# Performance work log

Measured on AMD Instinct MI355X. Metric: run time of the kernel, lower is better.

Reference implementation:

```python
import jax, jax.numpy as jnp
import numpy as np

NUM_EMBEDDINGS = 1024
EMBEDDING_DIM = 256

def setup_inputs() -> dict:
    key = jax.random.key(0)
    k1, k2 = jax.random.split(key)
    x = jax.random.normal(k1, (8, 16, 32, 32, EMBEDDING_DIM), dtype=jnp.float32)
    embeddings = jax.random.normal(k2, (NUM_EMBEDDINGS, EMBEDDING_DIM), dtype=jnp.float32)
    return {"x": x, "embeddings": embeddings}

def reference(x, embeddings):
    # Flatten all leading dims to tokens: [N, D]
    flat = x.reshape(-1, EMBEDDING_DIM)
    # Squared euclidean distances via ||a||^2 + ||b||^2 - 2 a.b  -> [N, K]
    sim = jnp.matmul(flat, embeddings.T)
    distances = (jnp.sum(flat * flat, axis=1, keepdims=True)
                 + jnp.sum(embeddings * embeddings, axis=1)
                 - 2.0 * sim)
    encoding_indices = jnp.argmin(distances, axis=1)  # [N]
    quantized = embeddings[encoding_indices].reshape(x.shape)
    # Perplexity from code usage histogram (mean of one-hot == normalized counts)
    counts = jnp.zeros((NUM_EMBEDDINGS,), dtype=jnp.float32).at[encoding_indices].add(1.0)
    avg_probs = counts / flat.shape[0]
    perplexity = jnp.exp(-jnp.sum(avg_probs * jnp.log(avg_probs + 1e-10)))
    return quantized, perplexity
```

## Files before the change

kernel.cpp:

```cpp
#include <hip/hip_runtime.h>
#include <math.h>
#include <stdint.h>

#define NTOK 131072
#define DIM  256
#define KEMB 1024

typedef _Float16 f16x8 __attribute__((ext_vector_type(8)));
typedef float    f32x4 __attribute__((ext_vector_type(4)));

#define FLAG_CAP 65536
#define FLAG_THR 8u

static __device__ __forceinline__ unsigned umin32(unsigned a, unsigned b){ return a<b?a:b; }
static __device__ __forceinline__ unsigned umax32(unsigned a, unsigned b){ return a>b?a:b; }

static __device__ __forceinline__ void gload_lds16(const void* g, void* l) {
    __builtin_amdgcn_global_load_lds(
        (const __attribute__((address_space(1))) unsigned int*)g,
        (__attribute__((address_space(3))) unsigned int*)l, 16, 0, 0);
}

static __device__ __forceinline__ void split_hl(const float4& f0, const float4& f1,
                                                f16x8& h, f16x8& l) {
    float v[8] = {f0.x, f0.y, f0.z, f0.w, f1.x, f1.y, f1.z, f1.w};
    #pragma unroll
    for (int e = 0; e < 8; ++e) {
        const _Float16 hi = (_Float16)v[e];
        h[e] = hi;
        l[e] = (_Float16)(v[e] - (float)hi);
    }
}

__global__ __launch_bounds__(64) void prep_kernel(const float* __restrict__ emb,
                                                  float* __restrict__ eNorm,
                                                  float* __restrict__ cst2,
                                                  unsigned* __restrict__ counts,
                                                  unsigned* __restrict__ flagCnt,
                                                  _Float16* __restrict__ img_hi,
                                                  _Float16* __restrict__ img_lo) {
    const int k = blockIdx.x;
    const int lane = threadIdx.x;
    const float4 v = *reinterpret_cast<const float4*>(emb + (size_t)k * DIM + lane * 4);
    float s = v.x * v.x + v.y * v.y + v.z * v.z + v.w * v.w;
    #pragma unroll
    for (int m = 32; m; m >>= 1) s += __shfl_xor(s, m, 64);
    if (lane == 0) {
        eNorm[k] = s;
        cst2[k]  = s + 512.0f;
        counts[k] = 0u;
        if (k == 0) *flagCnt = 0u;
    }
    if (lane < 32) {
        const int p = lane;
        const int sl = p ^ (k & 7);
        const float4 f0 = *reinterpret_cast<const float4*>(emb + (size_t)k * DIM + sl * 8);
        const float4 f1 = *reinterpret_cast<const float4*>(emb + (size_t)k * DIM + sl * 8 + 4);
        f16x8 h, l;
        split_hl(f0, f1, h, l);
        *reinterpret_cast<f16x8*>(img_hi + (size_t)k * 256 + p * 8) = h;
        *reinterpret_cast<f16x8*>(img_lo + (size_t)k * 256 + p * 8) = l;
    }
}

__global__ __launch_bounds__(256, 2) void vq_main(const float* __restrict__ x,
                                                  const float* __restrict__ emb,
                                                  const _Float16* __restrict__ img,
                                                  const float* __restrict__ cst2,
                                                  int* __restrict__ idxArr,
                                                  unsigned* __restrict__ counts,
                                                  unsigned* __restrict__ flagCnt,
                                                  unsigned* __restrict__ flagList,
                                                  float* __restrict__ out) {
    __shared__ char Bsh[4][2][8192];
    __shared__ float cst_s[1024];
    __shared__ int idx_s[256];

    const int tid  = threadIdx.x;
    const int wv   = tid >> 6;
    const int lane = tid & 63;
    const int g    = lane >> 4;
    const int c    = lane & 15;
    const int T0   = blockIdx.x * 256;
    const int T0w  = T0 + wv * 64;

    char* const ldsbase = &Bsh[wv][0][0];

    *reinterpret_cast<float4*>(&cst_s[tid * 4]) =
        *reinterpret_cast<const float4*>(&cst2[tid * 4]);

    {
        const char* src = (const char*)img + lane * 16;
        #pragma unroll
        for (int i = 0; i < 8; ++i)
            gload_lds16(src + i * 1024, ldsbase + i * 1024);
    }

    f16x8 a[4][8];
    #pragma unroll
    for (int i = 0; i < 4; ++i) {
        const float* xr = x + (size_t)(T0w + i * 16 + c) * DIM + g * 8;
        #pragma unroll
        for (int kk = 0; kk < 8; ++kk) {
            const float4 f0 = *reinterpret_cast<const float4*>(xr + kk * 32);
            const float4 f1 = *reinterpret_cast<const float4*>(xr + kk * 32 + 4);
            a[i][kk] = (f16x8){(_Float16)f0.x, (_Float16)f0.y, (_Float16)f0.z, (_Float16)f0.w,
                               (_Float16)f1.x, (_Float16)f1.y, (_Float16)f1.z, (_Float16)f1.w};
        }
    }

    unsigned m1[16], m2[16];
    #pragma unroll
    for (int t = 0; t < 16; ++t) { m1[t] = 0xFFFFFFFFu; m2[t] = 0xFFFFFFFFu; }

    __syncthreads();

#define ISSUE(NXT, ECN) do {                                                   \
        const char* _src = (const char*)img + (size_t)(ECN) * 8192 + lane * 16;\
        char* _dst = ldsbase + (NXT) * 8192;                                   \
        _Pragma("unroll")                                                      \
        for (int _i = 0; _i < 8; ++_i)                                         \
            gload_lds16(_src + _i * 1024, _dst + _i * 1024);                   \
    } while (0)

#define COMPUTE(CUR, EC) do {                                                  \
        const _Float16* _B = (const _Float16*)(ldsbase + (CUR) * 8192);        \
        const int   _col = (EC) * 16 + c;                                      \
        const float _cst = cst_s[_col];                                        \
        f32x4 _acc[4];                                                         \
        _Pragma("unroll")                                                      \
        for (int _i = 0; _i < 4; ++_i) _acc[_i] = (f32x4){0.f, 0.f, 0.f, 0.f}; \
        __builtin_amdgcn_s_setprio(1);                                         \
        _Pragma("unroll")                                                      \
        for (int _kk = 0; _kk < 8; ++_kk) {                                    \
            const f16x8 _b = *reinterpret_cast<const f16x8*>(                  \
                _B + c * 256 + (((_kk * 4 + g) ^ (c & 7)) << 3));              \
            _Pragma("unroll")                                                  \
            for (int _i = 0; _i < 4; ++_i)                                     \
                _acc[_i] = __builtin_amdgcn_mfma_f32_16x16x32_f16(             \
                    a[_i][_kk], _b, _acc[_i], 0, 0, 0);                        \
        }                                                                      \
        __builtin_amdgcn_s_setprio(0);                                         \
        _Pragma("unroll")                                                      \
        for (int _i = 0; _i < 4; ++_i)                                         \
            _Pragma("unroll")                                                  \
            for (int _e = 0; _e < 4; ++_e) {                                   \
                const float    _d = fmaf(_acc[_i][_e], -2.0f, _cst);           \
                const unsigned _k = (__builtin_bit_cast(unsigned, _d)          \
                                     & 0xFFFFFC00u) | (unsigned)_col;          \
                const int _t = _i * 4 + _e;                                    \
                m2[_t] = umin32(m2[_t], umax32(_k, m1[_t]));                   \
                m1[_t] = umin32(m1[_t], _k);                                   \
            }                                                                  \
    } while (0)

    for (int ec2 = 0; ec2 < 32; ++ec2) {
        const int ec0 = ec2 * 2;
        const int ec1 = ec0 + 1;

        ISSUE(1, ec0 + 1);
        asm volatile("s_waitcnt vmcnt(8)" ::: "memory");
        __builtin_amdgcn_sched_barrier(0);
        COMPUTE(0, ec0);

        if (ec1 < 63) {
            ISSUE(0, ec1 + 1);
            asm volatile("s_waitcnt vmcnt(8)" ::: "memory");
        } else {
            asm volatile("s_waitcnt vmcnt(0)" ::: "memory");
        }
        __builtin_amdgcn_sched_barrier(0);
        COMPUTE(1, ec1);
    }
#undef ISSUE
#undef COMPUTE

    #pragma unroll
    for (int off = 1; off < 16; off <<= 1) {
        #pragma unroll
        for (int t = 0; t < 16; ++t) {
            const unsigned o1 = __shfl_xor(m1[t], off, 64);
            const unsigned o2 = __shfl_xor(m2[t], off, 64);
            const unsigned nm2 = umin32(umin32(m2[t], o2), umax32(m1[t], o1));
            m1[t] = umin32(m1[t], o1);
            m2[t] = nm2;
        }
    }

    if (c == 0) {
        #pragma unroll
        for (int t = 0; t < 16; ++t) {
            const int i   = t >> 2;
            const int e   = t & 3;
            const int row = i * 16 + g * 4 + e;
            const int idx = (int)(m1[t] & 1023u);
            idx_s[wv * 64 + row] = idx;
            idxArr[T0w + row] = idx;
            atomicAdd(&counts[idx], 1u);
            if (((m2[t] >> 10) - (m1[t] >> 10)) < FLAG_THR) {
                const unsigned pos = atomicAdd(flagCnt, 1u);
                if (pos < FLAG_CAP) flagList[pos] = (unsigned)(T0w + row);
            }
        }
    }
    __syncthreads();

    #pragma unroll 4
    for (int s = 0; s < 64; ++s) {
        const int fi  = s * 256 + tid;
        const int row = fi >> 6;
        const int q4  = fi & 63;
        const int em  = idx_s[row];
        *reinterpret_cast<float4*>(out + (size_t)(T0 + row) * DIM + q4 * 4) =
            *reinterpret_cast<const float4*>(emb + (size_t)em * DIM + q4 * 4);
    }
}

__global__ __launch_bounds__(256) void fixup_refine(const float* __restrict__ x,
                                                    const _Float16* __restrict__ img_hi,
                                                    const _Float16* __restrict__ img_lo,
                                                    const float* __restrict__ cst2,
                                                    const unsigned* __restrict__ flagCnt,
                                                    const unsigned* __restrict__ flagList,
                                                    uint2* __restrict__ refTop) {
    __shared__ _Float16 Bh[16384];
    __shared__ _Float16 Bl[16384];
    __shared__ float cst_s[1024];

    const unsigned nf = umin32(*flagCnt, (unsigned)FLAG_CAP);
    if (blockIdx.x * 64u >= nf) return;

    const int tid  = threadIdx.x;
    const int wv   = tid >> 6;
    const int lane = tid & 63;
    const int g    = lane >> 4;
    const int c    = lane & 15;
    const unsigned base = (blockIdx.x * 4u + (unsigned)wv) * 16u;

    *reinterpret_cast<float4*>(&cst_s[tid * 4]) =
        *reinterpret_cast<const float4*>(&cst2[tid * 4]);

    const unsigned myTok = flagList[(base + c) < nf ? (base + c) : 0];
    f16x8 ah[8], al[8];
    {
        const float* xr = x + (size_t)myTok * DIM + g * 8;
        #pragma unroll
        for (int kk = 0; kk < 8; ++kk) {
            const float4 f0 = *reinterpret_cast<const float4*>(xr + kk * 32);
            const float4 f1 = *reinterpret_cast<const float4*>(xr + kk * 32 + 4);
            split_hl(f0, f1, ah[kk], al[kk]);
        }
    }

    unsigned m1[4], m2[4];
    #pragma unroll
    for (int e = 0; e < 4; ++e) { m1[e] = 0xFFFFFFFFu; m2[e] = 0xFFFFFFFFu; }

    for (int ec = 0; ec < 16; ++ec) {
        __syncthreads();
        #pragma unroll
        for (int i = 0; i < 8; ++i) {
            gload_lds16((const char*)img_hi + ec * 32768 + (i * 256 + tid) * 16,
                        (char*)&Bh[0] + i * 4096 + wv * 1024);
            gload_lds16((const char*)img_lo + ec * 32768 + (i * 256 + tid) * 16,
                        (char*)&Bl[0] + i * 4096 + wv * 1024);
        }
        __syncthreads();

        f32x4 acc[4];
        #pragma unroll
        for (int j = 0; j < 4; ++j) acc[j] = (f32x4){0.f, 0.f, 0.f, 0.f};

        #pragma unroll
        for (int kk = 0; kk < 8; ++kk) {
            #pragma unroll
            for (int j = 0; j < 4; ++j) {
                const int row = j * 16 + c;
                const int off = row * 256 + (((kk * 4 + g) ^ (row & 7)) << 3);
                const f16x8 bh = *reinterpret_cast<const f16x8*>(&Bh[off]);
                const f16x8 bl = *reinterpret_cast<const f16x8*>(&Bl[off]);
                acc[j] = __builtin_amdgcn_mfma_f32_16x16x32_f16(ah[kk], bh, acc[j], 0, 0, 0);
                acc[j] = __builtin_amdgcn_mfma_f32_16x16x32_f16(ah[kk], bl, acc[j], 0, 0, 0);
                acc[j] = __builtin_amdgcn_mfma_f32_16x16x32_f16(al[kk], bh, acc[j], 0, 0, 0);
            }
        }

        #pragma unroll
        for (int j = 0; j < 4; ++j) {
            const int   col = ec * 64 + j * 16 + c;
            const float cst = cst_s[col];
            #pragma unroll
            for (int e = 0; e < 4; ++e) {
                const float    d   = fmaf(acc[j][e], -2.0f, cst);
                const unsigned key = (__builtin_bit_cast(unsigned, d) & 0xFFFFFC00u) | (unsigned)col;
                m2[e] = umin32(m2[e], umax32(key, m1[e]));
                m1[e] = umin32(m1[e], key);
            }
        }
    }

    #pragma unroll
    for (int off = 1; off < 16; off <<= 1) {
        #pragma unroll
        for (int e = 0; e < 4; ++e) {
            const unsigned o1 = __shfl_xor(m1[e], off, 64);
            const unsigned o2 = __shfl_xor(m2[e], off, 64);
            const unsigned nm2 = umin32(umin32(m2[e], o2), umax32(m1[e], o1));
            m1[e] = umin32(m1[e], o1);
            m2[e] = nm2;
        }
    }

    if (c == 0) {
        #pragma unroll
        for (int e = 0; e < 4; ++e) {
            const unsigned pos = base + (unsigned)(g * 4 + e);
            if (pos < nf) refTop[pos] = make_uint2(m1[e], m2[e]);
        }
    }
}

__global__ __launch_bounds__(256) void fixup_exact(const float* __restrict__ x,
                                                   const float* __restrict__ emb,
                                                   const float* __restrict__ eNorm,
                                                   const unsigned* __restrict__ flagCnt,
                                                   const unsigned* __restrict__ flagList,
                                                   const uint2* __restrict__ refTop,
                                                   int* __restrict__ idxArr,
                                                   unsigned* __restrict__ counts,
                                                   float* __restrict__ out) {
    const unsigned nf = umin32(*flagCnt, (unsigned)FLAG_CAP);
    const int tid  = threadIdx.x;
    const int wv   = tid >> 6;
    const int lane = tid & 63;

    for (unsigned pos = blockIdx.x * 4u + (unsigned)wv; pos < nf; pos += gridDim.x * 4u) {
        const unsigned tok = flagList[pos];
        const uint2 tk = refTop[pos];
        const int e1 = (int)(tk.x & 1023u);
        const int e2 = (int)(tk.y & 1023u);

        const float4 xv = *reinterpret_cast<const float4*>(x   + (size_t)tok * DIM + lane * 4);
        const float4 v1 = *reinterpret_cast<const float4*>(emb + (size_t)e1  * DIM + lane * 4);
        const float4 v2 = *reinterpret_cast<const float4*>(emb + (size_t)e2  * DIM + lane * 4);
        float p1 = xv.x * v1.x + xv.y * v1.y + xv.z * v1.z + xv.w * v1.w;
        float p2 = xv.x * v2.x + xv.y * v2.y + xv.z * v2.z + xv.w * v2.w;
        #pragma unroll
        for (int off = 1; off < 64; off <<= 1) {
            p1 += __shfl_xor(p1, off, 64);
            p2 += __shfl_xor(p2, off, 64);
        }
        const float d1 = eNorm[e1] - 2.0f * p1;
        const float d2 = eNorm[e2] - 2.0f * p2;
        const bool pick2 = (d2 < d1) || (d2 == d1 && e2 < e1);
        const int  ni   = pick2 ? e2 : e1;
        const int  old  = idxArr[tok];
        if (ni != old) {
            if (lane == 0) {
                idxArr[tok] = ni;
                atomicSub(&counts[old], 1u);
                atomicAdd(&counts[ni], 1u);
            }
            const float4 nv = pick2 ? v2 : v1;
            *reinterpret_cast<float4*>(out + (size_t)tok * DIM + lane * 4) = nv;
        }
    }
}

__global__ __launch_bounds__(256) void perp_kernel(const unsigned* __restrict__ counts,
                                                   float* __restrict__ out_perp) {
    __shared__ float red[256];
    const int tid = threadIdx.x;
    float s = 0.0f;
    for (int i = tid; i < KEMB; i += 256) {
        const float p = (float)counts[i] / (float)NTOK;
        s += p * logf(p + 1e-10f);
    }
    red[tid] = s;
    __syncthreads();
    for (int off = 128; off; off >>= 1) {
        if (tid < off) red[tid] += red[tid + off];
        __syncthreads();
    }
    if (tid == 0) *out_perp = expf(-red[0]);
}

extern "C" void kernel_launch(void* const* d_in, const int* in_sizes, int n_in,
                              void* d_out, int out_size, void* d_ws, size_t ws_size,
                              hipStream_t stream) {
    (void)in_sizes; (void)n_in; (void)out_size; (void)ws_size;
    const float* x   = (const float*)d_in[0];
    const float* emb = (const float*)d_in[1];
    float* out = (float*)d_out;

    char* ws = (char*)d_ws;
    float*     eNorm    = (float*)(ws);
    float*     cst2     = (float*)(ws + 4096);
    unsigned*  counts   = (unsigned*)(ws + 8192);
    unsigned*  flagCnt  = (unsigned*)(ws + 12288);
    unsigned*  flagList = (unsigned*)(ws + 16384);
    int*       idxArr   = (int*)(ws + 278528);
    _Float16*  img_hi   = (_Float16*)(ws + 802816);
    _Float16*  img_lo   = (_Float16*)(ws + 1327104);
    uint2*     refTop   = (uint2*)(ws + 1851392);

    prep_kernel<<<KEMB, 64, 0, stream>>>(emb, eNorm, cst2, counts, flagCnt, img_hi, img_lo);
    vq_main<<<NTOK / 256, 256, 0, stream>>>(x, emb, img_hi, cst2, idxArr, counts,
                                            flagCnt, flagList, out);
    fixup_refine<<<1024, 256, 0, stream>>>(x, img_hi, img_lo, cst2, flagCnt, flagList, refTop);
    fixup_exact<<<2048, 256, 0, stream>>>(x, emb, eNorm, flagCnt, flagList, refTop,
                                          idxArr, counts, out);
    perp_kernel<<<1, 256, 0, stream>>>(counts, out + (size_t)NTOK * DIM);
}
```

Baseline: 206.5 us.

## Load codebook fragments directly into registers instead of staging through LDS

The prep kernel now writes an extra fp16 codebook image laid out in MFMA B-operand fragment order, so each lane reads its fragment with a coalesced 16-byte global load. The main kernel drops the LDS staging (global_load_lds double buffer, cst table in shared memory, syncthreads, explicit waitcnt and sched barriers and setprio) and double-buffers the B fragments in registers, reading the cst value from global memory. This removes LDS traffic and the manual pipeline, but adds register pressure and relies on the compiler and L2 cache to hide global-load latency.

```diff
diff --git a/kernel.cpp b/kernel.cpp
--- a/kernel.cpp
+++ b/kernel.cpp
@@ -38,7 +38,8 @@
                                                   unsigned* __restrict__ counts,
                                                   unsigned* __restrict__ flagCnt,
                                                   _Float16* __restrict__ img_hi,
-                                                  _Float16* __restrict__ img_lo) {
+                                                  _Float16* __restrict__ img_lo,
+                                                  _Float16* __restrict__ img2) {
     const int k = blockIdx.x;
     const int lane = threadIdx.x;
     const float4 v = *reinterpret_cast<const float4*>(emb + (size_t)k * DIM + lane * 4);
@@ -54,26 +55,31 @@
     if (lane < 32) {
         const int p = lane;
         const int sl = p ^ (k & 7);
-        const float4 f0 = *reinterpret_cast<const float4*>(emb + (size_t)k * DIM + sl * 8);
-        const float4 f1 = *reinterpret_cast<const float4*>(emb + (size_t)k * DIM + sl * 8 + 4);
+        const float4 s0 = *reinterpret_cast<const float4*>(emb + (size_t)k * DIM + sl * 8);
+        const float4 s1 = *reinterpret_cast<const float4*>(emb + (size_t)k * DIM + sl * 8 + 4);
         f16x8 h, l;
-        split_hl(f0, f1, h, l);
+        split_hl(s0, s1, h, l);
         *reinterpret_cast<f16x8*>(img_hi + (size_t)k * 256 + p * 8) = h;
         *reinterpret_cast<f16x8*>(img_lo + (size_t)k * 256 + p * 8) = l;
+        const int kk = p >> 2, g = p & 3;
+        const int ec = k >> 4, c = k & 15;
+        const float4 f0 = *reinterpret_cast<const float4*>(emb + (size_t)k * DIM + p * 8);
+        const float4 f1 = *reinterpret_cast<const float4*>(emb + (size_t)k * DIM + p * 8 + 4);
+        f16x8 h2, l2;
+        split_hl(f0, f1, h2, l2);
+        *reinterpret_cast<f16x8*>(img2 + (size_t)ec * 4096 + kk * 512 + (g * 16 + c) * 8) = h2;
     }
 }
 
 __global__ __launch_bounds__(256, 2) void vq_main(const float* __restrict__ x,
                                                   const float* __restrict__ emb,
-                                                  const _Float16* __restrict__ img,
+                                                  const _Float16* __restrict__ img2,
                                                   const float* __restrict__ cst2,
                                                   int* __restrict__ idxArr,
                                                   unsigned* __restrict__ counts,
                                                   unsigned* __restrict__ flagCnt,
                                                   unsigned* __restrict__ flagList,
                                                   float* __restrict__ out) {
-    __shared__ char Bsh[4][2][8192];
-    __shared__ float cst_s[1024];
     __shared__ int idx_s[256];
 
     const int tid  = threadIdx.x;
@@ -84,18 +90,6 @@
     const int T0   = blockIdx.x * 256;
     const int T0w  = T0 + wv * 64;
 
-    char* const ldsbase = &Bsh[wv][0][0];
-
-    *reinterpret_cast<float4*>(&cst_s[tid * 4]) =
-        *reinterpret_cast<const float4*>(&cst2[tid * 4]);
-
-    {
-        const char* src = (const char*)img + lane * 16;
-        #pragma unroll
-        for (int i = 0; i < 8; ++i)
-            gload_lds16(src + i * 1024, ldsbase + i * 1024);
-    }
-
     f16x8 a[4][8];
     #pragma unroll
     for (int i = 0; i < 4; ++i) {
@@ -113,39 +107,32 @@
     #pragma unroll
     for (int t = 0; t < 16; ++t) { m1[t] = 0xFFFFFFFFu; m2[t] = 0xFFFFFFFFu; }
 
-    __syncthreads();
-
-#define ISSUE(NXT, ECN) do {                                                   \
-        const char* _src = (const char*)img + (size_t)(ECN) * 8192 + lane * 16;\
-        char* _dst = ldsbase + (NXT) * 8192;                                   \
+    const _Float16* ibase = img2 + lane * 8;
+
+#define LOADB(DST, CSTD, EC) do {                                              \
         _Pragma("unroll")                                                      \
-        for (int _i = 0; _i < 8; ++_i)                                         \
-            gload_lds16(_src + _i * 1024, _dst + _i * 1024);                   \
+        for (int _kk = 0; _kk < 8; ++_kk)                                      \
+            DST[_kk] = *reinterpret_cast<const f16x8*>(                        \
+                ibase + (size_t)(EC) * 4096 + _kk * 512);                      \
+        CSTD = cst2[(EC) * 16 + c];                                            \
     } while (0)
 
-#define COMPUTE(CUR, EC) do {                                                  \
-        const _Float16* _B = (const _Float16*)(ldsbase + (CUR) * 8192);        \
-        const int   _col = (EC) * 16 + c;                                      \
-        const float _cst = cst_s[_col];                                        \
+#define COMPUTE(BUF, CST, EC) do {                                             \
         f32x4 _acc[4];                                                         \
         _Pragma("unroll")                                                      \
         for (int _i = 0; _i < 4; ++_i) _acc[_i] = (f32x4){0.f, 0.f, 0.f, 0.f}; \
-        __builtin_amdgcn_s_setprio(1);                                         \
         _Pragma("unroll")                                                      \
-        for (int _kk = 0; _kk < 8; ++_kk) {                                    \
-            const f16x8 _b = *reinterpret_cast<const f16x8*>(                  \
-                _B + c * 256 + (((_kk * 4 + g) ^ (c & 7)) << 3));              \
+        for (int _kk = 0; _kk < 8; ++_kk)                                      \
             _Pragma("unroll")                                                  \
             for (int _i = 0; _i < 4; ++_i)                                     \
                 _acc[_i] = __builtin_amdgcn_mfma_f32_16x16x32_f16(             \
-                    a[_i][_kk], _b, _acc[_i], 0, 0, 0);                        \
-        }                                                                      \
-        __builtin_amdgcn_s_setprio(0);                                         \
+                    a[_i][_kk], BUF[_kk], _acc[_i], 0, 0, 0);                  \
+        const int _col = (EC) * 16 + c;                                        \
         _Pragma("unroll")                                                      \
         for (int _i = 0; _i < 4; ++_i)                                         \
             _Pragma("unroll")                                                  \
             for (int _e = 0; _e < 4; ++_e) {                                   \
-                const float    _d = fmaf(_acc[_i][_e], -2.0f, _cst);           \
+                const float    _d = fmaf(_acc[_i][_e], -2.0f, CST);            \
                 const unsigned _k = (__builtin_bit_cast(unsigned, _d)          \
                                      & 0xFFFFFC00u) | (unsigned)_col;          \
                 const int _t = _i * 4 + _e;                                    \
@@ -154,25 +141,18 @@
             }                                                                  \
     } while (0)
 
+    f16x8 bA[8], bB[8];
+    float cstA, cstB;
+    LOADB(bA, cstA, 0);
+
     for (int ec2 = 0; ec2 < 32; ++ec2) {
         const int ec0 = ec2 * 2;
-        const int ec1 = ec0 + 1;
-
-        ISSUE(1, ec0 + 1);
-        asm volatile("s_waitcnt vmcnt(8)" ::: "memory");
-        __builtin_amdgcn_sched_barrier(0);
-        COMPUTE(0, ec0);
-
-        if (ec1 < 63) {
-            ISSUE(0, ec1 + 1);
-            asm volatile("s_waitcnt vmcnt(8)" ::: "memory");
-        } else {
-            asm volatile("s_waitcnt vmcnt(0)" ::: "memory");
-        }
-        __builtin_amdgcn_sched_barrier(0);
-        COMPUTE(1, ec1);
-    }
-#undef ISSUE
+        LOADB(bB, cstB, ec0 + 1);
+        COMPUTE(bA, cstA, ec0);
+        if (ec0 + 2 < 64) LOADB(bA, cstA, ec0 + 2);
+        COMPUTE(bB, cstB, ec0 + 1);
+    }
+#undef LOADB
 #undef COMPUTE
 
     #pragma unroll
@@ -403,9 +383,11 @@
     _Float16*  img_hi   = (_Float16*)(ws + 802816);
     _Float16*  img_lo   = (_Float16*)(ws + 1327104);
     uint2*     refTop   = (uint2*)(ws + 1851392);
-
-    prep_kernel<<<KEMB, 64, 0, stream>>>(emb, eNorm, cst2, counts, flagCnt, img_hi, img_lo);
-    vq_main<<<NTOK / 256, 256, 0, stream>>>(x, emb, img_hi, cst2, idxArr, counts,
+    _Float16*  img2     = (_Float16*)(ws + 2363392);
+
+    prep_kernel<<<KEMB, 64, 0, stream>>>(emb, eNorm, cst2, counts, flagCnt,
+                                         img_hi, img_lo, img2);
+    vq_main<<<NTOK / 256, 256, 0, stream>>>(x, emb, img2, cst2, idxArr, counts,
                                             flagCnt, flagList, out);
     fixup_refine<<<1024, 256, 0, stream>>>(x, img_hi, img_lo, cst2, flagCnt, flagList, refTop);
     fixup_exact<<<2048, 256, 0, stream>>>(x, emb, eNorm, flagCnt, flagList, refTop,
```

Result: no change. 207.2 us (+0.3%).
